# Kernel tuning notes

Hardware: AMD Instinct MI355X
Metric: run time of the kernel (lower is better)

## Reference

```python
import jax, jax.numpy as jnp
import numpy as np
from jax import lax

K = 3       # kernel_conv
STRIDE = 1
PAD = 1


def setup_inputs() -> dict:
    key = jax.random.key(0)
    ks = jax.random.split(key, 11)
    b, n, H, W = 8, 64, 128, 128
    m = 64
    kk = K * K
    return {
        "x": jax.random.normal(ks[0], (b, n, H, W), jnp.float32),
        "atw1": jax.random.uniform(ks[1], (b, kk, H, W), jnp.float32),  # sigmoid-range attention1 output
        "weight": jax.random.normal(ks[2], (m, n, K, K), jnp.float32) * 0.05,
        "a2_w1": jax.random.normal(ks[3], (kk, n), jnp.float32) * 0.1,
        "a2_b1": jax.random.normal(ks[4], (kk,), jnp.float32) * 0.1,
        "a2_w2": jax.random.normal(ks[5], (kk, kk), jnp.float32) * 0.1,
        "a2_b2": jax.random.normal(ks[6], (kk,), jnp.float32) * 0.1,
        "a3_w1": jax.random.normal(ks[7], (m, n), jnp.float32) * 0.1,
        "a3_b1": jax.random.normal(ks[8], (m,), jnp.float32) * 0.1,
        "a3_w2": jax.random.normal(ks[9], (m, m), jnp.float32) * 0.1,
        "a3_b2": jax.random.normal(ks[10], (m,), jnp.float32) * 0.1,
    }


def reference(x, atw1, weight, a2_w1, a2_b1, a2_w2, a2_b2, a3_w1, a3_b1, a3_w2, a3_b2):
    b, n, H, W = x.shape
    m = weight.shape[0]
    kk = K * K
    n_H = 1 + (H + 2 * PAD - K) // STRIDE
    n_W = 1 + (W + 2 * PAD - K) // STRIDE
    P = n_H * n_W

    # F.unfold(x, k, stride, padding): [b, n*k*k, P] with channel-major ordering (c, kh, kw)
    patches = lax.conv_general_dilated_patches(
        x, (K, K), (STRIDE, STRIDE), [(PAD, PAD), (PAD, PAD)])  # [b, n*kk, n_H, n_W]
    kx = patches.reshape(b, n, kk, P)

    # attention2: global avg pool + two 1x1 convs -> per-batch per-tap ratio [b, kk]
    g = x.mean(axis=(2, 3))                                   # [b, n]
    ratio = jax.nn.relu(g @ a2_w1.T + a2_b1) @ a2_w2.T + a2_b2  # [b, kk]

    # per-pixel per-tap weight (broadcast over input channels, as the torch repeat/view does)
    a = atw1.reshape(b, kk, P) * ratio[:, :, None]            # [b, kk, P]
    wx = kx * a[:, None, :, :]                                # [b, n, kk, P]

    # dynamic-weighted im2col matmul with static conv weight
    w = weight.reshape(m, n, kk)
    y = jnp.einsum('bctp,mct->bmp', wx, w)                    # [b, m, P]

    # attention3 bias: global avg pool + two 1x1 convs -> [b, m]
    bias = jax.nn.relu(g @ a3_w1.T + a3_b1) @ a3_w2.T + a3_b2
    y = y + bias[:, :, None]

    # F.fold with kernel 1 is a reshape back to the spatial grid
    return y.reshape(b, m, n_H, n_W)
```

## Files before the change

### kernel.cpp

```cpp
#include <hip/hip_runtime.h>

typedef __attribute__((ext_vector_type(8))) short short8;
typedef __attribute__((ext_vector_type(4))) float f32x4;

#define HH 128
#define WW 128
#define TW 16
#define TH 4
#define HALOW 18
#define HALOH 6
#define NPIX (HALOW * HALOH)
#define NA (9 * TH * TW)

typedef __attribute__((address_space(1))) const unsigned int glds_src_t;
typedef __attribute__((address_space(3))) unsigned int glds_dst_t;

__device__ inline unsigned short f2bf(float f) {
    unsigned int u = __builtin_bit_cast(unsigned int, f);
    u += 0x7fffu + ((u >> 16) & 1u);
    return (unsigned short)(u >> 16);
}

__global__ __launch_bounds__(256) void prep_kernel(
    const float* __restrict__ x, const float* __restrict__ wgt,
    unsigned short* __restrict__ xT, float* __restrict__ partials,
    unsigned short* __restrict__ W3, float* __restrict__ zpage) {
    const int id = blockIdx.x;
    const int tid = threadIdx.x;
    if (id == 0 && tid < 32) zpage[tid] = 0.f;
    {
        int i = id * 256 + tid;
        if (i < 64 * 64 * 9) {
            int j = i & 7, rest = i >> 3;
            int m = rest & 63; rest >>= 6;
            int lk = rest & 3; rest >>= 2;
            int ks = rest & 1, t = rest >> 1;
            int c = ks * 32 + lk * 8 + j;
            W3[i] = f2bf(wgt[(m * 64 + c) * 9 + t]);
        }
    }
    const int b = id & 7, pt = id >> 3;
    const int p0 = pt * 64;
    __shared__ unsigned int lt[64 * 33];
    __shared__ float red[8][32][2];

    const int px = tid & 63, cp0 = tid >> 6;
    const float* xb = x + (size_t)b * 64 * (HH * WW) + p0 + px;
    #pragma unroll
    for (int i = 0; i < 8; ++i) {
        int cp = cp0 + 4 * i;
        float v0 = xb[(size_t)(2 * cp) * (HH * WW)];
        float v1 = xb[(size_t)(2 * cp + 1) * (HH * WW)];
        lt[px * 33 + cp] = (unsigned)f2bf(v0) | ((unsigned)f2bf(v1) << 16);
    }
    __syncthreads();
    #pragma unroll
    for (int it = 0; it < 2; ++it) {
        int idx = it * 256 + tid;
        int p = idx >> 3, ch = idx & 7;
        int o = p * 33 + ch * 4;
        uint4 v = make_uint4(lt[o], lt[o + 1], lt[o + 2], lt[o + 3]);
        *(uint4*)(xT + ((size_t)(b * (HH * WW) + p0 + p) * 64 + ch * 8)) = v;
    }
    {
        int cp = tid & 31, grp = tid >> 5;
        float s0 = 0.f, s1 = 0.f;
        #pragma unroll
        for (int j2 = 0; j2 < 8; ++j2) {
            unsigned u = lt[(grp * 8 + j2) * 33 + cp];
            s0 += __builtin_bit_cast(float, u << 16);
            s1 += __builtin_bit_cast(float, u & 0xffff0000u);
        }
        red[grp][cp][0] = s0;
        red[grp][cp][1] = s1;
    }
    __syncthreads();
    if (tid < 64) {
        float s = 0.f;
        #pragma unroll
        for (int g2 = 0; g2 < 8; ++g2) s += red[g2][tid >> 1][tid & 1];
        partials[(size_t)(b * 256 + pt) * 64 + tid] = s;
    }
}

__global__ __launch_bounds__(256) void mlp_kernel(
    const float* __restrict__ partials,
    const float* __restrict__ a2w1, const float* __restrict__ a2b1,
    const float* __restrict__ a2w2, const float* __restrict__ a2b2,
    const float* __restrict__ a3w1, const float* __restrict__ a3b1,
    const float* __restrict__ a3w2, const float* __restrict__ a3b2,
    float* __restrict__ ratio, float* __restrict__ bias) {
    int b = blockIdx.x;
    int tid = threadIdx.x;
    int t = tid & 63, is = tid >> 6;
    float s = 0.f;
    #pragma unroll 8
    for (int k = 0; k < 64; ++k)
        s += partials[(size_t)(b * 256 + is + 4 * k) * 64 + t];
    __shared__ float rb[4][64];
    __shared__ float gs[64], h2[9], h3[64];
    rb[is][t] = s;
    __syncthreads();
    if (tid < 64)
        gs[t] = (rb[0][t] + rb[1][t] + rb[2][t] + rb[3][t]) * (1.f / (HH * WW));
    __syncthreads();
    if (tid < 64) {
        float s3 = 0.f;
        #pragma unroll 8
        for (int i = 0; i < 64; ++i) s3 += gs[i] * a3w1[t * 64 + i];
        h3[t] = fmaxf(s3 + a3b1[t], 0.f);
        if (t < 9) {
            float s2 = 0.f;
            #pragma unroll 8
            for (int i = 0; i < 64; ++i) s2 += gs[i] * a2w1[t * 64 + i];
            h2[t] = fmaxf(s2 + a2b1[t], 0.f);
        }
    }
    __syncthreads();
    if (tid < 64) {
        float o = 0.f;
        #pragma unroll 8
        for (int i = 0; i < 64; ++i) o += h3[i] * a3w2[t * 64 + i];
        bias[b * 64 + t] = o + a3b2[t];
        if (t < 9) {
            float r = 0.f;
            #pragma unroll
            for (int i = 0; i < 9; ++i) r += h2[i] * a2w2[t * 9 + i];
            ratio[b * 9 + t] = r + a2b2[t];
        }
    }
}

__global__ __launch_bounds__(256, 2) void main_kernel(
    const unsigned short* __restrict__ xT, const float* __restrict__ atw1,
    const unsigned short* __restrict__ W3, const float* __restrict__ ratio,
    const float* __restrict__ bias, float* __restrict__ out,
    const float* __restrict__ zpage) {
    const int id = blockIdx.x;
    const int b = id & 7;
    const int j = id >> 3;
    const int tid = threadIdx.x;
    const int lane = tid & 63;
    const int wtile = tid >> 6;
    const int lm = lane & 15;
    const int lk = lane >> 4;

    __shared__ char xsc[2][16384];
    __shared__ float alds[2][768];

    short8 wfrag[9][2];
    {
        const short8* W3v = (const short8*)W3;
        #pragma unroll
        for (int t = 0; t < 9; ++t)
            #pragma unroll
            for (int ks = 0; ks < 2; ++ks)
                wfrag[t][ks] = W3v[(((t * 2 + ks) * 4 + lk) * 64) + wtile * 16 + lm];
    }
    float rat[9];
    #pragma unroll
    for (int t = 0; t < 9; ++t) rat[t] = ratio[b * 9 + t];
    float biasr[4];
    #pragma unroll
    for (int q = 0; q < 4; ++q) biasr[q] = bias[b * 64 + wtile * 16 + lk * 4 + q];

    const char* xbb = (const char*)(xT + (size_t)b * (HH * WW) * 64);
    const float* ab = atw1 + (size_t)b * 9 * (HH * WW);
    float* ob = out + (size_t)b * 64 * (HH * WW);
    const char* zp = (const char*)zpage;

    auto STAGE = [&](int bi, int task) {
        const int py0 = (task >> 3) * TH, px0 = (task & 7) * TW;
        #pragma unroll
        for (int i = 0; i < 4; ++i) {
            int idx = i * 256 + tid;
            int pix = idx >> 3, ch = idx & 7;
            int yy = pix / HALOW;
            int xx = pix - yy * HALOW;
            int gy = py0 + yy - 1, gx = px0 + xx - 1;
            bool ok = (pix < NPIX) && (gy >= 0) && (gy < HH) && (gx >= 0) && (gx < WW);
            const char* src = ok
                ? xbb + (((size_t)(gy * WW + gx)) << 7) + ((ch * 16) ^ ((pix & 7) << 4))
                : zp;
            char* dst = &xsc[bi][(i * 256 + wtile * 64) * 16];
            __builtin_amdgcn_global_load_lds((glds_src_t*)src, (glds_dst_t*)dst, 16, 0, 0);
        }
        #pragma unroll
        for (int i = 0; i < 3; ++i) {
            int idx = i * 256 + tid;
            int t = idx >> 6, rem = idx & 63;
            int rr = rem >> 4, cc = rem & 15;
            bool ok = idx < NA;
            const char* src = ok
                ? (const char*)(ab + (size_t)t * (HH * WW) + (py0 + rr) * WW + px0 + cc)
                : zp;
            float* dst = &alds[bi][i * 256 + wtile * 64];
            __builtin_amdgcn_global_load_lds((glds_src_t*)src, (glds_dst_t*)dst, 4, 0, 0);
        }
    };

    STAGE(0, j * 4);
    __syncthreads();

    #pragma unroll 1
    for (int it = 0; it < 4; ++it) {
        if (it < 3) STAGE((it + 1) & 1, j * 4 + it + 1);

        const int task = j * 4 + it;
        const int py0 = (task >> 3) * TH, px0 = (task & 7) * TW;
        const char* xs = xsc[it & 1];
        const float* al = alds[it & 1];

        #pragma unroll
        for (int g2 = 0; g2 < 2; ++g2) {
            const int r0 = g2 * 2;
            float av[2][9];
            #pragma unroll
            for (int rr = 0; rr < 2; ++rr)
                #pragma unroll
                for (int t = 0; t < 9; ++t)
                    av[rr][t] = al[t * 64 + (r0 + rr) * 16 + lm] * rat[t];

            f32x4 yac[2];
            #pragma unroll
            for (int rr = 0; rr < 2; ++rr) yac[rr] = (f32x4){0.f, 0.f, 0.f, 0.f};

            #pragma unroll
            for (int hl = 0; hl < 4; ++hl) {
                const int pixr = (r0 + hl) * HALOW + lm;
                short8 bf[3][2];
                #pragma unroll
                for (int dx = 0; dx < 3; ++dx) {
                    const int pix = pixr + dx;
                    const int sw = (pix & 7) << 4;
                    const char* bp2 = xs + pix * 128;
                    #pragma unroll
                    for (int ks = 0; ks < 2; ++ks)
                        bf[dx][ks] = __builtin_bit_cast(short8,
                            *(const uint4*)(bp2 + ((ks * 64 + lk * 16) ^ sw)));
                }
                #pragma unroll
                for (int dy = 0; dy < 3; ++dy) {
                    const int r = hl - dy;
                    if (r < 0 || r > 1) continue;
                    #pragma unroll
                    for (int dx = 0; dx < 3; ++dx) {
                        const int t = dy * 3 + dx;
                        f32x4 z = {0.f, 0.f, 0.f, 0.f};
                        z = __builtin_amdgcn_mfma_f32_16x16x32_bf16(wfrag[t][0], bf[dx][0], z, 0, 0, 0);
                        z = __builtin_amdgcn_mfma_f32_16x16x32_bf16(wfrag[t][1], bf[dx][1], z, 0, 0, 0);
                        #pragma unroll
                        for (int q = 0; q < 4; ++q) yac[r][q] = fmaf(av[r][t], z[q], yac[r][q]);
                    }
                }
            }
            #pragma unroll
            for (int rr = 0; rr < 2; ++rr) {
                const int pyg = py0 + r0 + rr;
                #pragma unroll
                for (int q = 0; q < 4; ++q) {
                    int m = wtile * 16 + lk * 4 + q;
                    ob[((size_t)m * HH + pyg) * WW + px0 + lm] = yac[rr][q] + biasr[q];
                }
            }
        }

        __syncthreads();
    }
}

extern "C" void kernel_launch(void* const* d_in, const int* in_sizes, int n_in,
                              void* d_out, int out_size, void* d_ws, size_t ws_size,
                              hipStream_t stream) {
    const float* x    = (const float*)d_in[0];
    const float* atw1 = (const float*)d_in[1];
    const float* wgt  = (const float*)d_in[2];
    const float* a2w1 = (const float*)d_in[3];
    const float* a2b1 = (const float*)d_in[4];
    const float* a2w2 = (const float*)d_in[5];
    const float* a2b2 = (const float*)d_in[6];
    const float* a3w1 = (const float*)d_in[7];
    const float* a3b1 = (const float*)d_in[8];
    const float* a3w2 = (const float*)d_in[9];
    const float* a3b2 = (const float*)d_in[10];
    float* out = (float*)d_out;

    float* ws = (float*)d_ws;
    float* ratio = ws;
    float* bias  = ws + 128;
    float* zpage = ws + 640;
    unsigned short* W3 = (unsigned short*)(ws + 1024);
    float* partials = ws + 19456;
    unsigned short* xT = (unsigned short*)(ws + 150528);

    prep_kernel<<<dim3(2048), dim3(256), 0, stream>>>(x, wgt, xT, partials, W3, zpage);
    mlp_kernel<<<dim3(8), dim3(256), 0, stream>>>(partials, a2w1, a2b1, a2w2, a2b2,
                                                  a3w1, a3b1, a3w2, a3b2, ratio, bias);
    main_kernel<<<dim3(512), dim3(256), 0, stream>>>(xT, atw1, W3, ratio, bias, out, zpage);
}
```

Measured before the change: 40.51 us.

## Fuse attention MLP into main kernel and relax loop-end barrier waits

```diff
diff --git a/kernel.cpp b/kernel.cpp
--- a/kernel.cpp
+++ b/kernel.cpp
@@ -83,59 +83,14 @@
     }
 }
 
-__global__ __launch_bounds__(256) void mlp_kernel(
-    const float* __restrict__ partials,
+__global__ __launch_bounds__(256, 2) void main_kernel(
+    const unsigned short* __restrict__ xT, const float* __restrict__ atw1,
+    const unsigned short* __restrict__ W3, const float* __restrict__ partials,
     const float* __restrict__ a2w1, const float* __restrict__ a2b1,
     const float* __restrict__ a2w2, const float* __restrict__ a2b2,
     const float* __restrict__ a3w1, const float* __restrict__ a3b1,
     const float* __restrict__ a3w2, const float* __restrict__ a3b2,
-    float* __restrict__ ratio, float* __restrict__ bias) {
-    int b = blockIdx.x;
-    int tid = threadIdx.x;
-    int t = tid & 63, is = tid >> 6;
-    float s = 0.f;
-    #pragma unroll 8
-    for (int k = 0; k < 64; ++k)
-        s += partials[(size_t)(b * 256 + is + 4 * k) * 64 + t];
-    __shared__ float rb[4][64];
-    __shared__ float gs[64], h2[9], h3[64];
-    rb[is][t] = s;
-    __syncthreads();
-    if (tid < 64)
-        gs[t] = (rb[0][t] + rb[1][t] + rb[2][t] + rb[3][t]) * (1.f / (HH * WW));
-    __syncthreads();
-    if (tid < 64) {
-        float s3 = 0.f;
-        #pragma unroll 8
-        for (int i = 0; i < 64; ++i) s3 += gs[i] * a3w1[t * 64 + i];
-        h3[t] = fmaxf(s3 + a3b1[t], 0.f);
-        if (t < 9) {
-            float s2 = 0.f;
-            #pragma unroll 8
-            for (int i = 0; i < 64; ++i) s2 += gs[i] * a2w1[t * 64 + i];
-            h2[t] = fmaxf(s2 + a2b1[t], 0.f);
-        }
-    }
-    __syncthreads();
-    if (tid < 64) {
-        float o = 0.f;
-        #pragma unroll 8
-        for (int i = 0; i < 64; ++i) o += h3[i] * a3w2[t * 64 + i];
-        bias[b * 64 + t] = o + a3b2[t];
-        if (t < 9) {
-            float r = 0.f;
-            #pragma unroll
-            for (int i = 0; i < 9; ++i) r += h2[i] * a2w2[t * 9 + i];
-            ratio[b * 9 + t] = r + a2b2[t];
-        }
-    }
-}
-
-__global__ __launch_bounds__(256, 2) void main_kernel(
-    const unsigned short* __restrict__ xT, const float* __restrict__ atw1,
-    const unsigned short* __restrict__ W3, const float* __restrict__ ratio,
-    const float* __restrict__ bias, float* __restrict__ out,
-    const float* __restrict__ zpage) {
+    float* __restrict__ out, const float* __restrict__ zpage) {
     const int id = blockIdx.x;
     const int b = id & 7;
     const int j = id >> 3;
@@ -147,22 +102,8 @@
 
     __shared__ char xsc[2][16384];
     __shared__ float alds[2][768];
-
-    short8 wfrag[9][2];
-    {
-        const short8* W3v = (const short8*)W3;
-        #pragma unroll
-        for (int t = 0; t < 9; ++t)
-            #pragma unroll
-            for (int ks = 0; ks < 2; ++ks)
-                wfrag[t][ks] = W3v[(((t * 2 + ks) * 4 + lk) * 64) + wtile * 16 + lm];
-    }
-    float rat[9];
-    #pragma unroll
-    for (int t = 0; t < 9; ++t) rat[t] = ratio[b * 9 + t];
-    float biasr[4];
-    #pragma unroll
-    for (int q = 0; q < 4; ++q) biasr[q] = bias[b * 64 + wtile * 16 + lk * 4 + q];
+    __shared__ float rb[4][64];
+    __shared__ float gs[64], h3[64], h2[12], rrs[12], bbs[64];
 
     const char* xbb = (const char*)(xT + (size_t)b * (HH * WW) * 64);
     const float* ab = atw1 + (size_t)b * 9 * (HH * WW);
@@ -200,11 +141,69 @@
     };
 
     STAGE(0, j * 4);
-    __syncthreads();
+
+    short8 wfrag[9][2];
+    {
+        const short8* W3v = (const short8*)W3;
+        #pragma unroll
+        for (int t = 0; t < 9; ++t)
+            #pragma unroll
+            for (int ks = 0; ks < 2; ++ks)
+                wfrag[t][ks] = W3v[(((t * 2 + ks) * 4 + lk) * 64) + wtile * 16 + lm];
+    }
+
+    {
+        const int t = tid & 63, is = tid >> 6;
+        float s = 0.f;
+        #pragma unroll 8
+        for (int k = 0; k < 64; ++k)
+            s += partials[(size_t)(b * 256 + is + 4 * k) * 64 + t];
+        rb[is][t] = s;
+        __syncthreads();
+        if (tid < 64)
+            gs[t] = (rb[0][t] + rb[1][t] + rb[2][t] + rb[3][t]) * (1.f / (HH * WW));
+        __syncthreads();
+        if (tid < 64) {
+            float s3 = 0.f;
+            #pragma unroll 8
+            for (int i = 0; i < 64; ++i) s3 += gs[i] * a3w1[t * 64 + i];
+            h3[t] = fmaxf(s3 + a3b1[t], 0.f);
+            if (t < 9) {
+                float s2 = 0.f;
+                #pragma unroll 8
+                for (int i = 0; i < 64; ++i) s2 += gs[i] * a2w1[t * 64 + i];
+                h2[t] = fmaxf(s2 + a2b1[t], 0.f);
+            }
+        }
+        __syncthreads();
+        if (tid < 64) {
+            float o = 0.f;
+            #pragma unroll 8
+            for (int i = 0; i < 64; ++i) o += h3[i] * a3w2[t * 64 + i];
+            bbs[t] = o + a3b2[t];
+            if (t < 9) {
+                float r = 0.f;
+                #pragma unroll
+                for (int i = 0; i < 9; ++i) r += h2[i] * a2w2[t * 9 + i];
+                rrs[t] = r + a2b2[t];
+            }
+        }
+        __syncthreads();
+    }
+
+    float rat[9];
+    #pragma unroll
+    for (int t = 0; t < 9; ++t) rat[t] = rrs[t];
+    float biasr[4];
+    #pragma unroll
+    for (int q = 0; q < 4; ++q) biasr[q] = bbs[wtile * 16 + lk * 4 + q];
 
     #pragma unroll 1
     for (int it = 0; it < 4; ++it) {
-        if (it < 3) STAGE((it + 1) & 1, j * 4 + it + 1);
+        if (it < 3) {
+            STAGE((it + 1) & 1, j * 4 + it + 1);
+            __builtin_amdgcn_sched_barrier(0);
+        }
 
         const int task = j * 4 + it;
         const int py0 = (task >> 3) * TH, px0 = (task & 7) * TW;
@@ -265,7 +264,11 @@
             }
         }
 
-        __syncthreads();
+        if (it < 3) {
+            asm volatile("s_waitcnt vmcnt(16)" ::: "memory");
+            __builtin_amdgcn_s_barrier();
+            __builtin_amdgcn_sched_barrier(0);
+        }
     }
 }
 
@@ -286,15 +289,13 @@
     float* out = (float*)d_out;
 
     float* ws = (float*)d_ws;
-    float* ratio = ws;
-    float* bias  = ws + 128;
     float* zpage = ws + 640;
     unsigned short* W3 = (unsigned short*)(ws + 1024);
     float* partials = ws + 19456;
     unsigned short* xT = (unsigned short*)(ws + 150528);
 
     prep_kernel<<<dim3(2048), dim3(256), 0, stream>>>(x, wgt, xT, partials, W3, zpage);
-    mlp_kernel<<<dim3(8), dim3(256), 0, stream>>>(partials, a2w1, a2b1, a2w2, a2b2,
-                                                  a3w1, a3b1, a3w2, a3b2, ratio, bias);
-    main_kernel<<<dim3(512), dim3(256), 0, stream>>>(xT, atw1, W3, ratio, bias, out, zpage);
+    main_kernel<<<dim3(512), dim3(256), 0, stream>>>(
+        xT, atw1, W3, partials, a2w1, a2b1, a2w2, a2b2,
+        a3w1, a3b1, a3w2, a3b2, out, zpage);
 }
```

Result: faster. 37.83 us (-6.6%).
